# Kernel optimization log

Measured on AMD Instinct MI355X. Metric: run time of the kernel, lower is better.

## Reference

```python
import jax, jax.numpy as jnp
import numpy as np

N = 500_000      # total rows (e.g. video frames)
S = 10_000       # number of segments (shots)
D_IN = 128
D_OUT = 128


def setup_inputs() -> dict:
    key = jax.random.key(0)
    k1, k2, k3 = jax.random.split(key, 3)
    inp = jax.random.normal(k1, (N, D_IN), dtype=jnp.float32)
    # contiguous non-overlapping segments covering [0, N): graph[j] = (start_j, end_j) inclusive
    rng = np.random.default_rng(0)
    cuts = np.sort(rng.choice(np.arange(1, N), size=S - 1, replace=False))
    starts = np.concatenate([[0], cuts]).astype(np.int64)
    ends = np.concatenate([cuts - 1, [N - 1]]).astype(np.int64)
    graph = jnp.asarray(np.stack([starts, ends], axis=1))  # [S, 2]
    # nn.Linear params (kaiming-uniform-ish scale is irrelevant for correctness baseline)
    W = jax.random.normal(k2, (D_OUT, D_IN), dtype=jnp.float32) * (1.0 / np.sqrt(D_IN))
    b = jax.random.normal(k3, (D_OUT,), dtype=jnp.float32) * 0.01
    return {"input": inp, "graph": graph, "W": W, "b": b}


def reference(input, graph, W, b):
    # One big GEMM for the projection (instead of per-segment Linear calls) ...
    y = input @ W.T + b                              # [N, D_OUT]
    n = input.shape[0]
    s = graph.shape[0]
    starts = graph[:, 0]
    ends = graph[:, 1]
    rows = jnp.arange(n)
    # ... then a single irregular segment reduction over ragged boundaries.
    seg_id = jnp.clip(jnp.searchsorted(starts, rows, side="right") - 1, 0, s - 1)  # [N]
    valid = (rows >= starts[seg_id]) & (rows <= ends[seg_id])  # guards any uncovered rows
    y = jnp.where(valid[:, None], y, 0.0)
    return jax.ops.segment_sum(y, seg_id, num_segments=s)     # [S, D_OUT]
```

## Files before the change

### kernel.cpp

```cpp
#include <hip/hip_runtime.h>
#include <hip/hip_bf16.h>


#define D 128
#define D4 32
#define CHUNK 128

__device__ __forceinline__ void f4add(float4& a, const float4& v) {
  a.x += v.x; a.y += v.y; a.z += v.z; a.w += v.w;
}

__global__ __launch_bounds__(256) void zero_kernel(float4* __restrict__ Xs) {
  Xs[blockIdx.x * 256 + threadIdx.x] = make_float4(0.f, 0.f, 0.f, 0.f);
}

__global__ __launch_bounds__(256) void seg_sum_kernel(
    const float* __restrict__ in, const int* __restrict__ graph,
    float* __restrict__ Xs, int N, int S) {
  __shared__ float4 red[256];

  int tid = threadIdx.x;
  int rg  = tid >> 5;
  int c4  = tid & 31;

  int c0 = blockIdx.x * CHUNK;
  int c1 = min(c0 + CHUNK, N);

  int lo = 0, hi = S - 1;
  while (lo < hi) {
    int mid = (lo + hi + 1) >> 1;
    if (graph[2 * mid] <= c0) lo = mid; else hi = mid - 1;
  }

  for (int s = lo; s < S; ++s) {
    int rs = graph[2 * s];
    if (rs > c1 - 1) break;
    int re  = graph[2 * s + 1];
    int nxt = (s + 1 < S) ? (graph[2 * s + 2] - 1) : (N - 1);
    re = min(re, min(nxt, N - 1));
    rs = max(rs, 0);

    int rlo = max(rs, c0);
    int rhi = min(re, c1 - 1);
    if (rlo > rhi) continue;
    int cnt = rhi - rlo + 1;

    const float4* p = (const float4*)in + (size_t)rlo * D4 + c4;
    float4 a0 = make_float4(0.f, 0.f, 0.f, 0.f);
    float4 a1 = make_float4(0.f, 0.f, 0.f, 0.f);
    float4 a2 = make_float4(0.f, 0.f, 0.f, 0.f);
    float4 a3 = make_float4(0.f, 0.f, 0.f, 0.f);

    int r = rg;
    for (; r + 24 < cnt; r += 32) {
      float4 v0 = p[(r     ) * D4];
      float4 v1 = p[(r +  8) * D4];
      float4 v2 = p[(r + 16) * D4];
      float4 v3 = p[(r + 24) * D4];
      f4add(a0, v0); f4add(a1, v1); f4add(a2, v2); f4add(a3, v3);
    }
    for (; r < cnt; r += 8) {
      f4add(a0, p[r * D4]);
    }
    f4add(a0, a1); f4add(a2, a3); f4add(a0, a2);

    red[tid] = a0;
    __syncthreads();
    if (tid < 128) { f4add(red[tid], red[tid + 128]); }
    __syncthreads();
    if (tid < 64)  { f4add(red[tid], red[tid + 64]); }
    __syncthreads();
    if (tid < 32) {
      float4 r4 = red[tid];
      f4add(r4, red[tid + 32]);
      if (rs >= c0 && re <= c1 - 1) {
        ((float4*)Xs)[(size_t)s * D4 + tid] = r4;
      } else {
        float* dst = Xs + (size_t)s * D + tid * 4;
        atomicAdd(dst + 0, r4.x);
        atomicAdd(dst + 1, r4.y);
        atomicAdd(dst + 2, r4.z);
        atomicAdd(dst + 3, r4.w);
      }
    }
    __syncthreads();
  }
}

#define SEG_PB 16
#define OUT_PB 64
#define WT_STRIDE 65

__global__ __launch_bounds__(256) void seg_gemm_kernel(
    const float* __restrict__ Xs, const float* __restrict__ W,
    const float* __restrict__ b, const int* __restrict__ graph,
    float* __restrict__ out, int N, int S) {
  __shared__ float Wt[D * WT_STRIDE];
  __shared__ __align__(16) float XsL[SEG_PB * D];
  __shared__ float cntL[SEG_PB];

  int tid   = threadIdx.x;
  int s0    = blockIdx.x * SEG_PB;
  int oBase = blockIdx.y * OUT_PB;

  #pragma unroll
  for (int rnd = 0; rnd < 8; ++rnd) {
    int linear = rnd * 256 + tid;
    int op     = linear >> 5;
    int d4     = (linear & 31) << 2;
    float4 w = *(const float4*)(W + (oBase + op) * D + d4);
    Wt[(d4 + 0) * WT_STRIDE + op] = w.x;
    Wt[(d4 + 1) * WT_STRIDE + op] = w.y;
    Wt[(d4 + 2) * WT_STRIDE + op] = w.z;
    Wt[(d4 + 3) * WT_STRIDE + op] = w.w;
  }
  {
    const float4* src = (const float4*)(Xs + s0 * D);
    float4* dst = (float4*)XsL;
    dst[tid]       = src[tid];
    dst[tid + 256] = src[tid + 256];
  }
  if (tid < SEG_PB) {
    int s   = s0 + tid;
    int rs  = graph[2 * s];
    int re  = graph[2 * s + 1];
    int nxt = (s + 1 < S) ? (graph[2 * s + 2] - 1) : (N - 1);
    re = min(re, min(nxt, N - 1));
    rs = max(rs, 0);
    cntL[tid] = (float)max(0, re - rs + 1);
  }
  __syncthreads();

  int op = tid & 63;
  int g  = tid >> 6;
  float acc[4] = {0.f, 0.f, 0.f, 0.f};

  const float4* xs4 = (const float4*)XsL;
  #pragma unroll 8
  for (int d4 = 0; d4 < D4; ++d4) {
    float w0 = Wt[(4 * d4 + 0) * WT_STRIDE + op];
    float w1 = Wt[(4 * d4 + 1) * WT_STRIDE + op];
    float w2 = Wt[(4 * d4 + 2) * WT_STRIDE + op];
    float w3 = Wt[(4 * d4 + 3) * WT_STRIDE + op];
    #pragma unroll
    for (int j = 0; j < 4; ++j) {
      float4 x = xs4[(4 * j + g) * D4 + d4];
      acc[j] += x.x * w0 + x.y * w1 + x.z * w2 + x.w * w3;
    }
  }

  float bo = b[oBase + op];
  #pragma unroll
  for (int j = 0; j < 4; ++j) {
    int sl = 4 * j + g;
    out[(s0 + sl) * D + oBase + op] = acc[j] + cntL[sl] * bo;
  }
}

extern "C" void kernel_launch(void* const* d_in, const int* in_sizes, int n_in,
                              void* d_out, int out_size, void* d_ws, size_t ws_size,
                              hipStream_t stream) {
  const float* in    = (const float*)d_in[0];
  const int*   graph = (const int*)d_in[1];
  const float* W     = (const float*)d_in[2];
  const float* b     = (const float*)d_in[3];
  float* out = (float*)d_out;

  const int N = in_sizes[0] / D;
  const int S = in_sizes[1] / 2;

  float* Xs = (float*)d_ws;

  zero_kernel<<<(S * D4) / 256, 256, 0, stream>>>((float4*)Xs);

  int nChunks = (N + CHUNK - 1) / CHUNK;
  seg_sum_kernel<<<nChunks, 256, 0, stream>>>(in, graph, Xs, N, S);

  dim3 grid2(S / SEG_PB, D / OUT_PB);
  seg_gemm_kernel<<<grid2, 256, 0, stream>>>(Xs, W, b, graph, out, N, S);
}
```

Measured before the change: 375.7 us.

## Precompute chunk segment starts, double chunk size, use predicated loads and shuffle reduction

Moves the per-chunk binary search over segment starts into the zeroing kernel, which writes each chunk's first segment index to workspace. The segment-sum kernel reads that index and works on chunks twice as large. Its row loop becomes branch-free: row indices are clamped to the last valid row and the extra rows are masked by a 0/1 multiplier, so every iteration issues four loads. The block reduction now uses a cross-half wave shuffle plus one shared-memory stage, cutting the number of __syncthreads. The trade-offs are fewer blocks, which may lower occupancy, and redundant clamped loads on short segments.

```diff
diff --git a/kernel.cpp b/kernel.cpp
--- a/kernel.cpp
+++ b/kernel.cpp
@@ -4,35 +4,47 @@
 
 #define D 128
 #define D4 32
-#define CHUNK 128
+#define CHUNK 256
 
 __device__ __forceinline__ void f4add(float4& a, const float4& v) {
   a.x += v.x; a.y += v.y; a.z += v.z; a.w += v.w;
 }
-
-__global__ __launch_bounds__(256) void zero_kernel(float4* __restrict__ Xs) {
-  Xs[blockIdx.x * 256 + threadIdx.x] = make_float4(0.f, 0.f, 0.f, 0.f);
+__device__ __forceinline__ void f4fma(float4& a, float m, const float4& v) {
+  a.x += m * v.x; a.y += m * v.y; a.z += m * v.z; a.w += m * v.w;
+}
+
+__global__ __launch_bounds__(256) void zero_kernel(
+    float4* __restrict__ Xs, const int* __restrict__ graph,
+    int* __restrict__ chunkFirst, int S, int nChunks) {
+  int g = blockIdx.x * 256 + threadIdx.x;
+  Xs[g] = make_float4(0.f, 0.f, 0.f, 0.f);
+  if (g < nChunks) {
+    int c0 = g * CHUNK;
+    int lo = 0, hi = S - 1;
+    while (lo < hi) {
+      int mid = (lo + hi + 1) >> 1;
+      if (graph[2 * mid] <= c0) lo = mid; else hi = mid - 1;
+    }
+    chunkFirst[g] = lo;
+  }
 }
 
 __global__ __launch_bounds__(256) void seg_sum_kernel(
     const float* __restrict__ in, const int* __restrict__ graph,
-    float* __restrict__ Xs, int N, int S) {
-  __shared__ float4 red[256];
-
-  int tid = threadIdx.x;
-  int rg  = tid >> 5;
-  int c4  = tid & 31;
+    const int* __restrict__ chunkFirst, float* __restrict__ Xs,
+    int N, int S) {
+  __shared__ float4 redW[128];
+
+  int tid  = threadIdx.x;
+  int rg   = tid >> 5;
+  int c4   = tid & 31;
+  int wv   = tid >> 6;
+  int lane = tid & 63;
 
   int c0 = blockIdx.x * CHUNK;
   int c1 = min(c0 + CHUNK, N);
 
-  int lo = 0, hi = S - 1;
-  while (lo < hi) {
-    int mid = (lo + hi + 1) >> 1;
-    if (graph[2 * mid] <= c0) lo = mid; else hi = mid - 1;
-  }
-
-  for (int s = lo; s < S; ++s) {
+  for (int s = chunkFirst[blockIdx.x]; s < S; ++s) {
     int rs = graph[2 * s];
     if (rs > c1 - 1) break;
     int re  = graph[2 * s + 1];
@@ -51,28 +63,32 @@
     float4 a2 = make_float4(0.f, 0.f, 0.f, 0.f);
     float4 a3 = make_float4(0.f, 0.f, 0.f, 0.f);
 
-    int r = rg;
-    for (; r + 24 < cnt; r += 32) {
-      float4 v0 = p[(r     ) * D4];
-      float4 v1 = p[(r +  8) * D4];
-      float4 v2 = p[(r + 16) * D4];
-      float4 v3 = p[(r + 24) * D4];
-      f4add(a0, v0); f4add(a1, v1); f4add(a2, v2); f4add(a3, v3);
-    }
-    for (; r < cnt; r += 8) {
-      f4add(a0, p[r * D4]);
+    int cm = cnt - 1;
+    for (int base = 0; base < cnt; base += 32) {
+      int r0 = base + rg;
+      int r1 = r0 + 8, r2 = r0 + 16, r3 = r0 + 24;
+      float4 v0 = p[(size_t)min(r0, cm) * D4];
+      float4 v1 = p[(size_t)min(r1, cm) * D4];
+      float4 v2 = p[(size_t)min(r2, cm) * D4];
+      float4 v3 = p[(size_t)min(r3, cm) * D4];
+      f4fma(a0, (r0 <= cm) ? 1.f : 0.f, v0);
+      f4fma(a1, (r1 <= cm) ? 1.f : 0.f, v1);
+      f4fma(a2, (r2 <= cm) ? 1.f : 0.f, v2);
+      f4fma(a3, (r3 <= cm) ? 1.f : 0.f, v3);
     }
     f4add(a0, a1); f4add(a2, a3); f4add(a0, a2);
 
-    red[tid] = a0;
-    __syncthreads();
-    if (tid < 128) { f4add(red[tid], red[tid + 128]); }
-    __syncthreads();
-    if (tid < 64)  { f4add(red[tid], red[tid + 64]); }
+    a0.x += __shfl_xor(a0.x, 32);
+    a0.y += __shfl_xor(a0.y, 32);
+    a0.z += __shfl_xor(a0.z, 32);
+    a0.w += __shfl_xor(a0.w, 32);
+    if (lane < 32) redW[wv * 32 + lane] = a0;
     __syncthreads();
     if (tid < 32) {
-      float4 r4 = red[tid];
-      f4add(r4, red[tid + 32]);
+      float4 r4 = redW[tid];
+      f4add(r4, redW[32 + tid]);
+      f4add(r4, redW[64 + tid]);
+      f4add(r4, redW[96 + tid]);
       if (rs >= c0 && re <= c1 - 1) {
         ((float4*)Xs)[(size_t)s * D4 + tid] = r4;
       } else {
@@ -169,12 +185,15 @@
   const int N = in_sizes[0] / D;
   const int S = in_sizes[1] / 2;
 
-  float* Xs = (float*)d_ws;
-
-  zero_kernel<<<(S * D4) / 256, 256, 0, stream>>>((float4*)Xs);
+  float* Xs        = (float*)d_ws;
+  int*   chunkFirst = (int*)(Xs + (size_t)S * D);
 
   int nChunks = (N + CHUNK - 1) / CHUNK;
-  seg_sum_kernel<<<nChunks, 256, 0, stream>>>(in, graph, Xs, N, S);
+
+  zero_kernel<<<(S * D4) / 256, 256, 0, stream>>>(
+      (float4*)Xs, graph, chunkFirst, S, nChunks);
+
+  seg_sum_kernel<<<nChunks, 256, 0, stream>>>(in, graph, chunkFirst, Xs, N, S);
 
   dim3 grid2(S / SEG_PB, D / OUT_PB);
   seg_gemm_kernel<<<grid2, 256, 0, stream>>>(Xs, W, b, graph, out, N, S);
```

New measurement: 377.9 us. About the same (+0.6%).
